# Performance work log

Measured on AMD Instinct MI355X. Metric: run time of the kernel, lower is better.

The kernel has to match this reference:

```python
import jax, jax.numpy as jnp
import numpy as np

H = 256  # hidden size for both encoder and decoder

def gru_cell(x, h, Wih, Whh, bih, bhh):
    # PyTorch nn.GRU cell: gates ordered (r, z, n)
    gi = x @ Wih.T + bih            # [N, 3H]
    gh = h @ Whh.T + bhh            # [N, 3H]
    ir, iz, inn = jnp.split(gi, 3, axis=-1)
    hr, hz, hn = jnp.split(gh, 3, axis=-1)
    r = jax.nn.sigmoid(ir + hr)
    z = jax.nn.sigmoid(iz + hz)
    n = jnp.tanh(inn + r * hn)
    return (1.0 - z) * n + z * h


def setup_inputs() -> dict:
    key = jax.random.key(0)
    ks = jax.random.split(key, 16)
    s = 0.05
    inp = {
        'x': jax.random.normal(ks[0], (32768, 15, 4), jnp.float32),
        'enc_embed_W': jax.random.normal(ks[1], (H, 4), jnp.float32) * s,
        'enc_embed_b': jax.random.normal(ks[2], (H,), jnp.float32) * s,
        'enc_Wih': jax.random.normal(ks[3], (3 * H, H), jnp.float32) * s,
        'enc_Whh': jax.random.normal(ks[4], (3 * H, H), jnp.float32) * s,
        'enc_bih': jax.random.normal(ks[5], (3 * H,), jnp.float32) * s,
        'enc_bhh': jax.random.normal(ks[6], (3 * H,), jnp.float32) * s,
        'dec_embed_W': jax.random.normal(ks[7], (H, H), jnp.float32) * s,
        'dec_embed_b': jax.random.normal(ks[8], (H,), jnp.float32) * s,
        'dec_Wih': jax.random.normal(ks[9], (3 * H, H), jnp.float32) * s,
        'dec_Whh': jax.random.normal(ks[10], (3 * H, H), jnp.float32) * s,
        'dec_bih': jax.random.normal(ks[11], (3 * H,), jnp.float32) * s,
        'dec_bhh': jax.random.normal(ks[12], (3 * H,), jnp.float32) * s,
        'out_W': jax.random.normal(ks[13], (4, H), jnp.float32) * s,
        'out_b': jax.random.normal(ks[14], (4,), jnp.float32) * s,
        'pred_len': 45,
    }
    return inp


def reference(x, enc_embed_W, enc_embed_b, enc_Wih, enc_Whh, enc_bih, enc_bhh,
              dec_embed_W, dec_embed_b, dec_Wih, dec_Whh, dec_bih, dec_bhh,
              out_W, out_b, pred_len):
    N = x.shape[0]
    # enc_embed: Linear + ReLU
    traj_feats = jax.nn.relu(jnp.einsum('nti,hi->nth', x, enc_embed_W) + enc_embed_b)
    # Encoder GRU over time (batch_first); we only need the final hidden state.
    h0 = jnp.zeros((N, H), x.dtype)

    def enc_step(h, xt):
        h = gru_cell(xt, h, enc_Wih, enc_Whh, enc_bih, enc_bhh)
        return h, None

    h_enc, _ = jax.lax.scan(enc_step, h0, jnp.swapaxes(traj_feats, 0, 1))

    dec_in0 = jax.nn.relu(h_enc @ dec_embed_W.T + dec_embed_b)

    def dec_step(carry, _):
        h, dec_in = carry
        h = gru_cell(dec_in, h, dec_Wih, dec_Whh, dec_bih, dec_bhh)
        out_t = h @ out_W.T + out_b                     # [N, 4]
        dec_in = jax.nn.relu(h @ dec_embed_W.T + dec_embed_b)
        return (h, dec_in), out_t

    _, outs = jax.lax.scan(dec_step, (h_enc, dec_in0), None, length=pred_len)
    return jnp.swapaxes(outs, 0, 1)  # [N, pred_len, 4]
```

## Files before the change

kernel.cpp:

```cpp
#include <hip/hip_runtime.h>
#include <hip/hip_fp16.h>

#define HD    256
#define TENC  15
#define PLEN  45
#define MROW  64
#define NTHR  512
#define NBLK  (32768 / MROW)

typedef __attribute__((ext_vector_type(16))) float     f32x16;
typedef __attribute__((ext_vector_type(8)))  _Float16  f16x8;

#define MFMAH __builtin_amdgcn_mfma_f32_32x32x16_f16

__device__ __forceinline__ float fast_sig(float x) {
    float e = __builtin_amdgcn_exp2f(-1.44269504088896f * x);
    return __builtin_amdgcn_rcpf(1.f + e);
}
__device__ __forceinline__ float fast_tanh(float x) {
    float e = __builtin_amdgcn_exp2f(-2.88539008177793f * x);
    return (1.f - e) * __builtin_amdgcn_rcpf(1.f + e);
}

__global__ void xpose_w_kernel(const float* __restrict__ src,
                               _Float16* __restrict__ dst, int n_gcols) {
    int t = blockIdx.x * blockDim.x + threadIdx.x;
    if (t >= n_gcols * 32) return;
    int gcol = t >> 5, c8 = t & 31;
    int kk = c8 >> 1, hi = c8 & 1;
    const float* s = src + (size_t)gcol * HD + c8 * 8;
    int seg = gcol >> 8, gc = gcol & 255;
    size_t d = (size_t)seg * 65536 +
               ((size_t)(((gc >> 5) * 16 + kk) * 64 + hi * 32 + (gc & 31))) * 8;
    _Float16 v[8];
    #pragma unroll
    for (int e = 0; e < 8; ++e) v[e] = (_Float16)s[e];
    *(f16x8*)(dst + d) = *(f16x8*)v;
}

__global__ void xpose_ow_kernel(const float* __restrict__ src,
                                _Float16* __restrict__ dst) {
    int t = blockIdx.x * blockDim.x + threadIdx.x;
    if (t >= 32 * 32) return;
    int gcol = t >> 5, c8 = t & 31;
    int kk = c8 >> 1, hi = c8 & 1;
    _Float16 v[8];
    if (gcol < 4) {
        const float* s = src + (size_t)gcol * HD + c8 * 8;
        #pragma unroll
        for (int e = 0; e < 8; ++e) v[e] = (_Float16)s[e];
    } else {
        #pragma unroll
        for (int e = 0; e < 8; ++e) v[e] = (_Float16)0.f;
    }
    size_t d = ((size_t)(kk * 64 + hi * 32 + gcol)) * 8;
    *(f16x8*)(dst + d) = *(f16x8*)v;
}

__device__ __forceinline__ int swz(int row, int col) {
    return row * 512 + ((((col >> 3) ^ row) & 31) << 4) + ((col & 7) << 1);
}

__global__ __launch_bounds__(NTHR, 2) void gru_main(
    const float* __restrict__ x,
    const float* __restrict__ eW, const float* __restrict__ eb,
    const _Float16* __restrict__ encWih, const _Float16* __restrict__ encWhh,
    const float* __restrict__ enc_bih, const float* __restrict__ enc_bhh,
    const _Float16* __restrict__ decEW, const float* __restrict__ dec_eb,
    const _Float16* __restrict__ decWih, const _Float16* __restrict__ decWhh,
    const float* __restrict__ dec_bih, const float* __restrict__ dec_bhh,
    const _Float16* __restrict__ outWt, const float* __restrict__ outb,
    float* __restrict__ out)
{
    __shared__ __align__(16) char ls_a[2][MROW * 512];
    __shared__ __align__(16) char ls_h[2][MROW * 512];
    __shared__ float ls_ew[HD * 4];
    __shared__ float ls_eb[HD];
    __shared__ float ls_bias[4 * HD];
    __shared__ float ls_deb[HD];

    const int tid   = threadIdx.x;
    const int lane  = tid & 63;
    const int wv    = tid >> 6;
    const int rowA  = lane & 31;
    const int hi    = lane >> 5;
    const int col   = wv * 32 + rowA;
    const int nbase = blockIdx.x * MROW;

    for (int i = tid; i < HD * 4; i += NTHR) ls_ew[i] = eW[i];
    if (tid < HD) {
        ls_eb[tid]            = eb[tid];
        ls_bias[tid]          = enc_bih[tid] + enc_bhh[tid];
        ls_bias[HD + tid]     = enc_bih[HD + tid] + enc_bhh[HD + tid];
        ls_bias[2 * HD + tid] = enc_bih[2 * HD + tid];
        ls_bias[3 * HD + tid] = enc_bhh[2 * HD + tid];
    }
    for (int i = tid; i < MROW * 512 / 4; i += NTHR) ((unsigned int*)ls_h[0])[i] = 0u;

    __half2 hpk[16];
    #pragma unroll
    for (int i = 0; i < 16; ++i) hpk[i] = __floats2half2_rn(0.f, 0.f);

    float bR, bZ, bN, bH;
    float deb, bb;

    f32x16 accR0, accR1, accZ0, accZ1, accN10, accN11, accN20, accN21;

    auto bcast = [](float v) {
        f32x16 a;
        #pragma unroll
        for (int i = 0; i < 16; ++i) a[i] = v;
        return a;
    };

    auto gates = [&](const _Float16* Wi, const _Float16* Wh, int ar, int hr) {
        accR0 = bcast(bR);  accR1 = accR0;
        accZ0 = bcast(bZ);  accZ1 = accZ0;
        accN10 = bcast(bN); accN11 = accN10;
        accN20 = bcast(bH); accN21 = accN20;
        const char* pA = ls_a[ar] + rowA * 512;
        const char* pH = ls_h[hr] + rowA * 512;
        const _Float16* bi = Wi + wv * 8192 + lane * 8;
        const _Float16* bh = Wh + wv * 8192 + lane * 8;
        #pragma unroll 2
        for (int kk = 0; kk < 16; ++kk) {
            const int sh = (((kk * 2 + hi) ^ rowA) & 31) << 4;
            f16x8 ax0 = *(const f16x8*)(pA + sh);
            f16x8 ax1 = *(const f16x8*)(pA + 16384 + sh);
            f16x8 ah0 = *(const f16x8*)(pH + sh);
            f16x8 ah1 = *(const f16x8*)(pH + 16384 + sh);
            const _Float16* ki = bi + kk * 512;
            const _Float16* kh = bh + kk * 512;
            f16x8 bri = *(const f16x8*)(ki);
            f16x8 bzi = *(const f16x8*)(ki + 65536);
            f16x8 bni = *(const f16x8*)(ki + 131072);
            f16x8 brh = *(const f16x8*)(kh);
            f16x8 bzh = *(const f16x8*)(kh + 65536);
            f16x8 bnh = *(const f16x8*)(kh + 131072);
            accR0  = MFMAH(ax0, bri, accR0, 0, 0, 0);
            accR1  = MFMAH(ax1, bri, accR1, 0, 0, 0);
            accZ0  = MFMAH(ax0, bzi, accZ0, 0, 0, 0);
            accZ1  = MFMAH(ax1, bzi, accZ1, 0, 0, 0);
            accN10 = MFMAH(ax0, bni, accN10, 0, 0, 0);
            accN11 = MFMAH(ax1, bni, accN11, 0, 0, 0);
            accR0  = MFMAH(ah0, brh, accR0, 0, 0, 0);
            accR1  = MFMAH(ah1, brh, accR1, 0, 0, 0);
            accZ0  = MFMAH(ah0, bzh, accZ0, 0, 0, 0);
            accZ1  = MFMAH(ah1, bzh, accZ1, 0, 0, 0);
            accN20 = MFMAH(ah0, bnh, accN20, 0, 0, 0);
            accN21 = MFMAH(ah1, bnh, accN21, 0, 0, 0);
        }
    };

    auto upd_tile = [&](f32x16& aR, f32x16& aZ, f32x16& aN1, f32x16& aN2, int rt) {
        #pragma unroll
        for (int q = 0; q < 16; q += 2) {
            float2 hv = __half22float2(hpk[rt * 8 + (q >> 1)]);
            float r0 = fast_sig(aR[q]);
            float z0 = fast_sig(aZ[q]);
            float n0 = fast_tanh(fmaf(r0, aN2[q], aN1[q]));
            float h0 = fmaf(z0, hv.x - n0, n0);
            float r1 = fast_sig(aR[q + 1]);
            float z1 = fast_sig(aZ[q + 1]);
            float n1 = fast_tanh(fmaf(r1, aN2[q + 1], aN1[q + 1]));
            float h1 = fmaf(z1, hv.y - n1, n1);
            hpk[rt * 8 + (q >> 1)] = __floats2half2_rn(h0, h1);
        }
    };

    auto write_h = [&](int hw) {
        #pragma unroll
        for (int rt = 0; rt < 2; ++rt)
            #pragma unroll
            for (int q = 0; q < 16; q += 2) {
                unsigned int u = *(unsigned int*)&hpk[rt * 8 + (q >> 1)];
                int row = rt * 32 + (q & 3) + ((q >> 2) << 3) + (hi << 2);
                *(unsigned short*)(ls_h[hw] + swz(row, col))     = (unsigned short)u;
                *(unsigned short*)(ls_h[hw] + swz(row + 1, col)) = (unsigned short)(u >> 16);
            }
    };

    auto embed_step = [&](int t, int aw) {
        int row = tid & 63;
        int c0  = (tid >> 6) * 32;
        const float4 xv = *(const float4*)(x + ((size_t)(nbase + row) * TENC + t) * 4);
        #pragma unroll 8
        for (int j = 0; j < 32; ++j) {
            int c = c0 + j;
            const float* wp = &ls_ew[c * 4];
            float v = fmaf(xv.x, wp[0], fmaf(xv.y, wp[1],
                      fmaf(xv.z, wp[2], fmaf(xv.w, wp[3], ls_eb[c]))));
            *(_Float16*)(ls_a[aw] + swz(row, c)) = (_Float16)fmaxf(v, 0.f);
        }
    };

    auto dec_embed = [&](int hr, int aw) {
        f32x16 o0 = bcast(deb), o1 = o0;
        const char* pH = ls_h[hr] + rowA * 512;
        const _Float16* be = decEW + wv * 8192 + lane * 8;
        #pragma unroll 2
        for (int kk = 0; kk < 16; ++kk) {
            const int sh = (((kk * 2 + hi) ^ rowA) & 31) << 4;
            f16x8 a0 = *(const f16x8*)(pH + sh);
            f16x8 a1 = *(const f16x8*)(pH + 16384 + sh);
            f16x8 b = *(const f16x8*)(be + kk * 512);
            o0 = MFMAH(a0, b, o0, 0, 0, 0);
            o1 = MFMAH(a1, b, o1, 0, 0, 0);
        }
        #pragma unroll
        for (int rt = 0; rt < 2; ++rt) {
            const f32x16& o = rt ? o1 : o0;
            #pragma unroll
            for (int q = 0; q < 16; ++q) {
                int row = rt * 32 + (q & 3) + ((q >> 2) << 3) + (hi << 2);
                *(_Float16*)(ls_a[aw] + swz(row, col)) = (_Float16)fmaxf(o[q], 0.f);
            }
        }
    };

    auto out_layer = [&](int t, int hr) {
        if ((wv & 3) == 0) {
            const int rt = wv >> 2;
            f32x16 o = bcast(bb);
            const char* pH = ls_h[hr] + rowA * 512 + rt * 16384;
            const _Float16* bo = outWt + lane * 8;
            #pragma unroll 2
            for (int kk = 0; kk < 16; ++kk) {
                const int sh = (((kk * 2 + hi) ^ rowA) & 31) << 4;
                f16x8 a = *(const f16x8*)(pH + sh);
                f16x8 b = *(const f16x8*)(bo + kk * 512);
                o = MFMAH(a, b, o, 0, 0, 0);
            }
            if (rowA < 4) {
                #pragma unroll
                for (int q = 0; q < 16; ++q) {
                    int row = rt * 32 + (q & 3) + ((q >> 2) << 3) + (hi << 2);
                    out[((size_t)(nbase + row) * PLEN + t) * 4 + rowA] = o[q];
                }
            }
        }
    };

    __syncthreads();
    bR = ls_bias[col];
    bZ = ls_bias[HD + col];
    bN = ls_bias[2 * HD + col];
    bH = ls_bias[3 * HD + col];
    embed_step(0, 0);
    __syncthreads();

    int ac = 0, hc = 0;

    for (int t = 0; t < TENC; ++t) {
        gates(encWih, encWhh, ac, hc);
        upd_tile(accR0, accZ0, accN10, accN20, 0);
        upd_tile(accR1, accZ1, accN11, accN21, 1);
        write_h(hc ^ 1);
        if (t + 1 < TENC) embed_step(t + 1, ac ^ 1);
        __syncthreads();
        ac ^= 1; hc ^= 1;
    }

    if (tid < HD) {
        ls_bias[tid]          = dec_bih[tid] + dec_bhh[tid];
        ls_bias[HD + tid]     = dec_bih[HD + tid] + dec_bhh[HD + tid];
        ls_bias[2 * HD + tid] = dec_bih[2 * HD + tid];
        ls_bias[3 * HD + tid] = dec_bhh[2 * HD + tid];
        ls_deb[tid]           = dec_eb[tid];
    }
    __syncthreads();
    bR = ls_bias[col];
    bZ = ls_bias[HD + col];
    bN = ls_bias[2 * HD + col];
    bH = ls_bias[3 * HD + col];
    deb = ls_deb[col];
    bb  = (rowA < 4) ? outb[rowA] : 0.f;
    ac = 0;
    dec_embed(hc, ac);
    __syncthreads();

    for (int t = 0; t < PLEN; ++t) {
        gates(decWih, decWhh, ac, hc);
        upd_tile(accR0, accZ0, accN10, accN20, 0);
        upd_tile(accR1, accZ1, accN11, accN21, 1);
        write_h(hc ^ 1);
        __syncthreads();
        dec_embed(hc ^ 1, ac ^ 1);
        __syncthreads();
        out_layer(t, hc ^ 1);
        ac ^= 1; hc ^= 1;
    }
}

extern "C" void kernel_launch(void* const* d_in, const int* in_sizes, int n_in,
                              void* d_out, int out_size, void* d_ws, size_t ws_size,
                              hipStream_t stream) {
    const float* x       = (const float*)d_in[0];
    const float* eW      = (const float*)d_in[1];
    const float* eb      = (const float*)d_in[2];
    const float* encWihf = (const float*)d_in[3];
    const float* encWhhf = (const float*)d_in[4];
    const float* enc_bih = (const float*)d_in[5];
    const float* enc_bhh = (const float*)d_in[6];
    const float* decEWf  = (const float*)d_in[7];
    const float* dec_eb  = (const float*)d_in[8];
    const float* decWihf = (const float*)d_in[9];
    const float* decWhhf = (const float*)d_in[10];
    const float* dec_bih = (const float*)d_in[11];
    const float* dec_bhh = (const float*)d_in[12];
    const float* outW    = (const float*)d_in[13];
    const float* outb    = (const float*)d_in[14];

    _Float16* ws = (_Float16*)d_ws;
    _Float16* hWih_e = ws;
    _Float16* hWhh_e = ws + 196608;
    _Float16* hWih_d = ws + 2 * 196608;
    _Float16* hWhh_d = ws + 3 * 196608;
    _Float16* hEW_d  = ws + 4 * 196608;
    _Float16* hOWt   = ws + 4 * 196608 + 65536;

    const int t1 = 768 * 32;
    const int t2 = 256 * 32;
    xpose_w_kernel<<<(t1 + 255) / 256, 256, 0, stream>>>(encWihf, hWih_e, 768);
    xpose_w_kernel<<<(t1 + 255) / 256, 256, 0, stream>>>(encWhhf, hWhh_e, 768);
    xpose_w_kernel<<<(t1 + 255) / 256, 256, 0, stream>>>(decWihf, hWih_d, 768);
    xpose_w_kernel<<<(t1 + 255) / 256, 256, 0, stream>>>(decWhhf, hWhh_d, 768);
    xpose_w_kernel<<<(t2 + 255) / 256, 256, 0, stream>>>(decEWf,  hEW_d,  256);
    xpose_ow_kernel<<<4, 256, 0, stream>>>(outW, hOWt);

    gru_main<<<NBLK, NTHR, 0, stream>>>(
        x, eW, eb, hWih_e, hWhh_e, enc_bih, enc_bhh,
        hEW_d, dec_eb, hWih_d, hWhh_d, dec_bih, dec_bhh,
        hOWt, outb, (float*)d_out);
}
```

Baseline: 2.297 ms.

## Split row tiles across twice as many waves per block

Doubles the block to 1024 threads so each wave handles a single 32-row tile rather than two. This halves per-wave accumulators and hidden-state registers and raises resident waves for latency hiding. In exchange, each weight fragment fetched from global memory feeds only one MFMA tile, doubling weight load traffic per block. Embedding, decoder embed, and output layer work are redistributed accordingly.

New measurement: 4.245 ms. 84.8% more time.

```diff
diff --git a/kernel.cpp b/kernel.cpp
--- a/kernel.cpp
+++ b/kernel.cpp
@@ -5,7 +5,7 @@
 #define TENC  15
 #define PLEN  45
 #define MROW  64
-#define NTHR  512
+#define NTHR  1024
 #define NBLK  (32768 / MROW)
 
 typedef __attribute__((ext_vector_type(16))) float     f32x16;
@@ -61,7 +61,7 @@
     return row * 512 + ((((col >> 3) ^ row) & 31) << 4) + ((col & 7) << 1);
 }
 
-__global__ __launch_bounds__(NTHR, 2) void gru_main(
+__global__ __launch_bounds__(NTHR, 4) void gru_main(
     const float* __restrict__ x,
     const float* __restrict__ eW, const float* __restrict__ eb,
     const _Float16* __restrict__ encWih, const _Float16* __restrict__ encWhh,
@@ -82,9 +82,11 @@
     const int tid   = threadIdx.x;
     const int lane  = tid & 63;
     const int wv    = tid >> 6;
+    const int w7    = wv & 7;
+    const int rh    = wv >> 3;
     const int rowA  = lane & 31;
     const int hi    = lane >> 5;
-    const int col   = wv * 32 + rowA;
+    const int col   = w7 * 32 + rowA;
     const int nbase = blockIdx.x * MROW;
 
     for (int i = tid; i < HD * 4; i += NTHR) ls_ew[i] = eW[i];
@@ -97,14 +99,14 @@
     }
     for (int i = tid; i < MROW * 512 / 4; i += NTHR) ((unsigned int*)ls_h[0])[i] = 0u;
 
-    __half2 hpk[16];
+    __half2 hpk[8];
     #pragma unroll
-    for (int i = 0; i < 16; ++i) hpk[i] = __floats2half2_rn(0.f, 0.f);
+    for (int i = 0; i < 8; ++i) hpk[i] = __floats2half2_rn(0.f, 0.f);
 
     float bR, bZ, bN, bH;
     float deb, bb;
 
-    f32x16 accR0, accR1, accZ0, accZ1, accN10, accN11, accN20, accN21;
+    f32x16 accR, accZ, accN1, accN2;
 
     auto bcast = [](float v) {
         f32x16 a;
@@ -114,21 +116,19 @@
     };
 
     auto gates = [&](const _Float16* Wi, const _Float16* Wh, int ar, int hr) {
-        accR0 = bcast(bR);  accR1 = accR0;
-        accZ0 = bcast(bZ);  accZ1 = accZ0;
-        accN10 = bcast(bN); accN11 = accN10;
-        accN20 = bcast(bH); accN21 = accN20;
-        const char* pA = ls_a[ar] + rowA * 512;
-        const char* pH = ls_h[hr] + rowA * 512;
-        const _Float16* bi = Wi + wv * 8192 + lane * 8;
-        const _Float16* bh = Wh + wv * 8192 + lane * 8;
+        accR  = bcast(bR);
+        accZ  = bcast(bZ);
+        accN1 = bcast(bN);
+        accN2 = bcast(bH);
+        const char* pA = ls_a[ar] + rowA * 512 + rh * 16384;
+        const char* pH = ls_h[hr] + rowA * 512 + rh * 16384;
+        const _Float16* bi = Wi + w7 * 8192 + lane * 8;
+        const _Float16* bh = Wh + w7 * 8192 + lane * 8;
         #pragma unroll 2
         for (int kk = 0; kk < 16; ++kk) {
             const int sh = (((kk * 2 + hi) ^ rowA) & 31) << 4;
-            f16x8 ax0 = *(const f16x8*)(pA + sh);
-            f16x8 ax1 = *(const f16x8*)(pA + 16384 + sh);
-            f16x8 ah0 = *(const f16x8*)(pH + sh);
-            f16x8 ah1 = *(const f16x8*)(pH + 16384 + sh);
+            f16x8 ax = *(const f16x8*)(pA + sh);
+            f16x8 ah = *(const f16x8*)(pH + sh);
             const _Float16* ki = bi + kk * 512;
             const _Float16* kh = bh + kk * 512;
             f16x8 bri = *(const f16x8*)(ki);
@@ -137,55 +137,47 @@
             f16x8 brh = *(const f16x8*)(kh);
             f16x8 bzh = *(const f16x8*)(kh + 65536);
             f16x8 bnh = *(const f16x8*)(kh + 131072);
-            accR0  = MFMAH(ax0, bri, accR0, 0, 0, 0);
-            accR1  = MFMAH(ax1, bri, accR1, 0, 0, 0);
-            accZ0  = MFMAH(ax0, bzi, accZ0, 0, 0, 0);
-            accZ1  = MFMAH(ax1, bzi, accZ1, 0, 0, 0);
-            accN10 = MFMAH(ax0, bni, accN10, 0, 0, 0);
-            accN11 = MFMAH(ax1, bni, accN11, 0, 0, 0);
-            accR0  = MFMAH(ah0, brh, accR0, 0, 0, 0);
-            accR1  = MFMAH(ah1, brh, accR1, 0, 0, 0);
-            accZ0  = MFMAH(ah0, bzh, accZ0, 0, 0, 0);
-            accZ1  = MFMAH(ah1, bzh, accZ1, 0, 0, 0);
-            accN20 = MFMAH(ah0, bnh, accN20, 0, 0, 0);
-            accN21 = MFMAH(ah1, bnh, accN21, 0, 0, 0);
-        }
-    };
-
-    auto upd_tile = [&](f32x16& aR, f32x16& aZ, f32x16& aN1, f32x16& aN2, int rt) {
+            accR  = MFMAH(ax, bri, accR, 0, 0, 0);
+            accZ  = MFMAH(ax, bzi, accZ, 0, 0, 0);
+            accN1 = MFMAH(ax, bni, accN1, 0, 0, 0);
+            accR  = MFMAH(ah, brh, accR, 0, 0, 0);
+            accZ  = MFMAH(ah, bzh, accZ, 0, 0, 0);
+            accN2 = MFMAH(ah, bnh, accN2, 0, 0, 0);
+        }
+    };
+
+    auto final_upd = [&]() {
         #pragma unroll
         for (int q = 0; q < 16; q += 2) {
-            float2 hv = __half22float2(hpk[rt * 8 + (q >> 1)]);
-            float r0 = fast_sig(aR[q]);
-            float z0 = fast_sig(aZ[q]);
-            float n0 = fast_tanh(fmaf(r0, aN2[q], aN1[q]));
+            float2 hv = __half22float2(hpk[q >> 1]);
+            float r0 = fast_sig(accR[q]);
+            float z0 = fast_sig(accZ[q]);
+            float n0 = fast_tanh(fmaf(r0, accN2[q], accN1[q]));
             float h0 = fmaf(z0, hv.x - n0, n0);
-            float r1 = fast_sig(aR[q + 1]);
-            float z1 = fast_sig(aZ[q + 1]);
-            float n1 = fast_tanh(fmaf(r1, aN2[q + 1], aN1[q + 1]));
+            float r1 = fast_sig(accR[q + 1]);
+            float z1 = fast_sig(accZ[q + 1]);
+            float n1 = fast_tanh(fmaf(r1, accN2[q + 1], accN1[q + 1]));
             float h1 = fmaf(z1, hv.y - n1, n1);
-            hpk[rt * 8 + (q >> 1)] = __floats2half2_rn(h0, h1);
+            hpk[q >> 1] = __floats2half2_rn(h0, h1);
         }
     };
 
     auto write_h = [&](int hw) {
         #pragma unroll
-        for (int rt = 0; rt < 2; ++rt)
-            #pragma unroll
-            for (int q = 0; q < 16; q += 2) {
-                unsigned int u = *(unsigned int*)&hpk[rt * 8 + (q >> 1)];
-                int row = rt * 32 + (q & 3) + ((q >> 2) << 3) + (hi << 2);
-                *(unsigned short*)(ls_h[hw] + swz(row, col))     = (unsigned short)u;
-                *(unsigned short*)(ls_h[hw] + swz(row + 1, col)) = (unsigned short)(u >> 16);
-            }
+        for (int q = 0; q < 16; q += 2) {
+            unsigned int u = *(unsigned int*)&hpk[q >> 1];
+            int row = rh * 32 + (q & 3) + ((q >> 2) << 3) + (hi << 2);
+            *(unsigned short*)(ls_h[hw] + swz(row, col))     = (unsigned short)u;
+            *(unsigned short*)(ls_h[hw] + swz(row + 1, col)) = (unsigned short)(u >> 16);
+        }
     };
 
     auto embed_step = [&](int t, int aw) {
         int row = tid & 63;
-        int c0  = (tid >> 6) * 32;
+        int c0  = (tid >> 6) * 16;
         const float4 xv = *(const float4*)(x + ((size_t)(nbase + row) * TENC + t) * 4);
-        #pragma unroll 8
-        for (int j = 0; j < 32; ++j) {
+        #pragma unroll 4
+        for (int j = 0; j < 16; ++j) {
             int c = c0 + j;
             const float* wp = &ls_ew[c * 4];
             float v = fmaf(xv.x, wp[0], fmaf(xv.y, wp[1],
@@ -195,34 +187,27 @@
     };
 
     auto dec_embed = [&](int hr, int aw) {
-        f32x16 o0 = bcast(deb), o1 = o0;
-        const char* pH = ls_h[hr] + rowA * 512;
-        const _Float16* be = decEW + wv * 8192 + lane * 8;
+        f32x16 o = bcast(deb);
+        const char* pH = ls_h[hr] + rowA * 512 + rh * 16384;
+        const _Float16* be = decEW + w7 * 8192 + lane * 8;
         #pragma unroll 2
         for (int kk = 0; kk < 16; ++kk) {
             const int sh = (((kk * 2 + hi) ^ rowA) & 31) << 4;
-            f16x8 a0 = *(const f16x8*)(pH + sh);
-            f16x8 a1 = *(const f16x8*)(pH + 16384 + sh);
+            f16x8 a = *(const f16x8*)(pH + sh);
             f16x8 b = *(const f16x8*)(be + kk * 512);
-            o0 = MFMAH(a0, b, o0, 0, 0, 0);
-            o1 = MFMAH(a1, b, o1, 0, 0, 0);
-        }
-        #pragma unroll
-        for (int rt = 0; rt < 2; ++rt) {
-            const f32x16& o = rt ? o1 : o0;
-            #pragma unroll
-            for (int q = 0; q < 16; ++q) {
-                int row = rt * 32 + (q & 3) + ((q >> 2) << 3) + (hi << 2);
-                *(_Float16*)(ls_a[aw] + swz(row, col)) = (_Float16)fmaxf(o[q], 0.f);
-            }
+            o = MFMAH(a, b, o, 0, 0, 0);
+        }
+        #pragma unroll
+        for (int q = 0; q < 16; ++q) {
+            int row = rh * 32 + (q & 3) + ((q >> 2) << 3) + (hi << 2);
+            *(_Float16*)(ls_a[aw] + swz(row, col)) = (_Float16)fmaxf(o[q], 0.f);
         }
     };
 
     auto out_layer = [&](int t, int hr) {
-        if ((wv & 3) == 0) {
-            const int rt = wv >> 2;
+        if (w7 == 0) {
             f32x16 o = bcast(bb);
-            const char* pH = ls_h[hr] + rowA * 512 + rt * 16384;
+            const char* pH = ls_h[hr] + rowA * 512 + rh * 16384;
             const _Float16* bo = outWt + lane * 8;
             #pragma unroll 2
             for (int kk = 0; kk < 16; ++kk) {
@@ -234,7 +219,7 @@
             if (rowA < 4) {
                 #pragma unroll
                 for (int q = 0; q < 16; ++q) {
-                    int row = rt * 32 + (q & 3) + ((q >> 2) << 3) + (hi << 2);
+                    int row = rh * 32 + (q & 3) + ((q >> 2) << 3) + (hi << 2);
                     out[((size_t)(nbase + row) * PLEN + t) * 4 + rowA] = o[q];
                 }
             }
@@ -253,8 +238,7 @@
 
     for (int t = 0; t < TENC; ++t) {
         gates(encWih, encWhh, ac, hc);
-        upd_tile(accR0, accZ0, accN10, accN20, 0);
-        upd_tile(accR1, accZ1, accN11, accN21, 1);
+        final_upd();
         write_h(hc ^ 1);
         if (t + 1 < TENC) embed_step(t + 1, ac ^ 1);
         __syncthreads();
@@ -281,8 +265,7 @@
 
     for (int t = 0; t < PLEN; ++t) {
         gates(decWih, decWhh, ac, hc);
-        upd_tile(accR0, accZ0, accN10, accN20, 0);
-        upd_tile(accR1, accZ1, accN11, accN21, 1);
+        final_upd();
         write_h(hc ^ 1);
         __syncthreads();
         dec_embed(hc ^ 1, ac ^ 1);
```
